# Kernel tuning notes

Hardware: AMD Instinct MI355X
Metric: run time of the kernel (lower is better)

## Reference

```python
import jax, jax.numpy as jnp
import numpy as np

# Sampled-neighborhood cascade sizes (src->dst per layer) and edge counts
N0, N1, N2, N3 = 400000, 200000, 100000, 50000
E1, E2, E3 = 500000, 300000, 150000
DIN, DH = 128, 128


def setup_inputs() -> dict:
    key = jax.random.key(0)
    ks = jax.random.split(key, 24)
    inp = {}
    inp['x'] = jax.random.normal(ks[0], (N0, DIN), jnp.float32)
    inp['src1'] = jax.random.randint(ks[1], (E1,), 0, N0, dtype=jnp.int64)
    inp['dst1'] = jax.random.randint(ks[2], (E1,), 0, N1, dtype=jnp.int64)
    inp['src2'] = jax.random.randint(ks[3], (E2,), 0, N1, dtype=jnp.int64)
    inp['dst2'] = jax.random.randint(ks[4], (E2,), 0, N2, dtype=jnp.int64)
    inp['src3'] = jax.random.randint(ks[5], (E3,), 0, N2, dtype=jnp.int64)
    inp['dst3'] = jax.random.randint(ks[6], (E3,), 0, N3, dtype=jnp.int64)
    # SAGEConv params: lin_l (on aggregated neighbors, with bias), lin_r (root, no bias)
    dims = [(DIN, DH), (DH, DH), (DH, DH)]
    for i, (di, do) in enumerate(dims, start=1):
        s = 1.0 / np.sqrt(di)
        inp[f'Wl{i}'] = jax.random.uniform(ks[6 + 4 * i - 3], (di, do), jnp.float32, -s, s)
        inp[f'Wr{i}'] = jax.random.uniform(ks[6 + 4 * i - 2], (di, do), jnp.float32, -s, s)
        inp[f'b{i}'] = jax.random.uniform(ks[6 + 4 * i - 1], (do,), jnp.float32, -s, s)
        inp[f'a{i}'] = jnp.full((do,), 0.25, jnp.float32)  # PReLU per-channel init
    return inp


def _sage_prelu(x_src, n_dst, src, dst, Wl, Wr, b, alpha):
    # mean aggregation over incoming edges (PyG SAGEConv default aggr='mean')
    x_dst = x_src[:n_dst]                                   # [n_dst, d]
    msg = x_src[src]                                        # [E, d] gather
    summed = jax.ops.segment_sum(msg, dst, num_segments=n_dst)
    cnt = jax.ops.segment_sum(jnp.ones(src.shape[0], x_src.dtype), dst,
                              num_segments=n_dst)
    mean = summed / jnp.maximum(cnt, 1.0)[:, None]
    out = mean @ Wl + b + x_dst @ Wr                        # lin_l(aggr) + lin_r(root)
    return jnp.where(out > 0, out, alpha * out)             # per-channel PReLU


def reference(x, src1, dst1, src2, dst2, src3, dst3,
              Wl1, Wr1, b1, a1, Wl2, Wr2, b2, a2, Wl3, Wr3, b3, a3):
    h = _sage_prelu(x, N1, src1, dst1, Wl1, Wr1, b1, a1)
    h = _sage_prelu(h, N2, src2, dst2, Wl2, Wr2, b2, a2)
    h = _sage_prelu(h, N3, src3, dst3, Wl3, Wr3, b3, a3)
    return h  # [N3, DH]
```

## Files before the change

### kernel.cpp

```cpp
#include <hip/hip_runtime.h>


constexpr int cN0 = 400000, cN1 = 200000, cN2 = 100000, cN3 = 50000;
constexpr int cE1 = 500000, cE2 = 300000, cE3 = 150000;
constexpr int cNT = cN1 + cN2 + cN3;
constexpr int cET = cE1 + cE2 + cE3;

#define NDIV_UP(a, b) (((a) + (b) - 1) / (b))

typedef __attribute__((ext_vector_type(8))) short bf16x8;
typedef __attribute__((ext_vector_type(4))) float f32x4;
typedef __attribute__((ext_vector_type(4))) unsigned u32x4;

__device__ __forceinline__ unsigned fbits(float f) {
  return __builtin_bit_cast(unsigned, f);
}
__device__ __forceinline__ float ffrom(unsigned u) {
  return __builtin_bit_cast(float, u);
}
__device__ __forceinline__ unsigned short f2bf(float f) {
  unsigned u = fbits(f);
  unsigned r = u + 0x7FFFu + ((u >> 16) & 1u);
  return (unsigned short)(r >> 16);
}

__global__ void detect_idx64_kernel(const long long* __restrict__ p, int E,
                                    long long nmax, int* __restrict__ flag) {
  int t = threadIdx.x;
  int n = E < 512 ? E : 512;
  int bad = 0;
  for (int i = t; i < n; i += 64) {
    long long v = p[i];
    if (v < 0 || v >= nmax) bad = 1;
  }
  unsigned long long b = __ballot(bad);
  if (t == 0) *flag = (b == 0ull) ? 1 : 0;
}

__device__ __forceinline__ int load_idx(const void* p, int i, int flag) {
  return flag ? (int)((const long long*)p)[i] : ((const int*)p)[i];
}

constexpr int NBLK_CH = NDIV_UP(cET, 256);

__global__ __launch_bounds__(256) void convhistpack_kernel(
    const float* __restrict__ x, unsigned short* __restrict__ xb,
    const void* __restrict__ d1, const void* __restrict__ d2,
    const void* __restrict__ d3, const int* __restrict__ flag,
    int* __restrict__ CNT,
    const float* __restrict__ Wl1, const float* __restrict__ Wr1,
    const float* __restrict__ Wl2, const float* __restrict__ Wr2,
    const float* __restrict__ Wl3, const float* __restrict__ Wr3,
    unsigned short* __restrict__ wpk) {
  const int bid = blockIdx.x;
  const int tid = threadIdx.x;
  const int gidx = bid * 256 + tid;

  if (gidx < cET) {
    const int f = *flag;
    int d;
    if (gidx < cE1) d = load_idx(d1, gidx, f);
    else if (gidx < cE1 + cE2) d = cN1 + load_idx(d2, gidx - cE1, f);
    else d = cN1 + cN2 + load_idx(d3, gidx - cE1 - cE2, f);
    atomicAdd(&CNT[d], 1);
  }

  {
    const int total4 = cN0 * 128 / 4;
    const int stride = NBLK_CH * 256;
    for (int i = gidx; i < total4; i += stride) {
      const float4 v = ((const float4*)x)[i];
      uint2 o;
      o.x = (unsigned)f2bf(v.x) | ((unsigned)f2bf(v.y) << 16);
      o.y = (unsigned)f2bf(v.z) | ((unsigned)f2bf(v.w) << 16);
      ((uint2*)xb)[i] = o;
    }
  }

  if (gidx < 3 * 16384) {
    const int L = gidx >> 14;
    const int r = gidx & 16383;
    const float* Wl = L == 0 ? Wl1 : (L == 1 ? Wl2 : Wl3);
    const float* Wr = L == 0 ? Wr1 : (L == 1 ? Wr2 : Wr3);
    unsigned short* o = wpk + L * 32768;
    const int j = r & 7, l = (r >> 3) & 63, cf = (r >> 9) & 7, ks = r >> 12;
    const int k = ks * 32 + (l >> 4) * 8 + j;
    const int col = cf * 16 + (l & 15);
    o[r] = f2bf(Wl[k * 128 + col]);
    o[16384 + r] = f2bf(Wr[k * 128 + col]);
  }
}

__global__ __launch_bounds__(256) void scan_reduce(const int* __restrict__ cnt,
                                                   int n, int* __restrict__ bsum) {
  __shared__ int s[256];
  int t = threadIdx.x;
  int base = blockIdx.x * 1024 + t * 4;
  int v = 0;
  if (base + 3 < n) {
    int4 c = *(const int4*)(cnt + base);
    v = c.x + c.y + c.z + c.w;
  } else {
    for (int i = 0; i < 4; ++i)
      if (base + i < n) v += cnt[base + i];
  }
  s[t] = v;
  __syncthreads();
  for (int off = 128; off > 0; off >>= 1) {
    if (t < off) s[t] += s[t + off];
    __syncthreads();
  }
  if (t == 0) bsum[blockIdx.x] = s[0];
}

__global__ __launch_bounds__(256) void scan_bsums(int* __restrict__ bsum, int nb) {
  __shared__ int s[256];
  int t = threadIdx.x;
  int v0 = (2 * t < nb) ? bsum[2 * t] : 0;
  int v1 = (2 * t + 1 < nb) ? bsum[2 * t + 1] : 0;
  int p = v0 + v1;
  s[t] = p;
  __syncthreads();
  for (int off = 1; off < 256; off <<= 1) {
    int x = (t >= off) ? s[t - off] : 0;
    __syncthreads();
    s[t] += x;
    __syncthreads();
  }
  int excl = s[t] - p;
  if (2 * t < nb) bsum[2 * t] = excl;
  if (2 * t + 1 < nb) bsum[2 * t + 1] = excl + v0;
}

__global__ __launch_bounds__(256) void scan_final(const int* __restrict__ cnt,
                                                  int n, const int* __restrict__ bsum,
                                                  int* __restrict__ offs) {
  __shared__ int s[256];
  int t = threadIdx.x;
  int base = blockIdx.x * 1024 + t * 4;
  int v0 = 0, v1 = 0, v2 = 0, v3 = 0;
  if (base + 3 < n) {
    int4 c = *(const int4*)(cnt + base);
    v0 = c.x; v1 = c.y; v2 = c.z; v3 = c.w;
  } else {
    if (base + 0 < n) v0 = cnt[base + 0];
    if (base + 1 < n) v1 = cnt[base + 1];
    if (base + 2 < n) v2 = cnt[base + 2];
  }
  int tsum = v0 + v1 + v2 + v3;
  s[t] = tsum;
  __syncthreads();
  for (int off = 1; off < 256; off <<= 1) {
    int x = (t >= off) ? s[t - off] : 0;
    __syncthreads();
    s[t] += x;
    __syncthreads();
  }
  int excl = s[t] - tsum;
  int o = bsum[blockIdx.x] + excl;
  if (base + 0 < n) offs[base + 0] = o;
  o += v0;
  if (base + 1 < n) offs[base + 1] = o;
  o += v1;
  if (base + 2 < n) offs[base + 2] = o;
  o += v2;
  if (base + 3 < n) offs[base + 3] = o;
}

__global__ void fill3_kernel(const void* __restrict__ s1, const void* __restrict__ d1,
                             const void* __restrict__ s2, const void* __restrict__ d2,
                             const void* __restrict__ s3, const void* __restrict__ d3,
                             const int* __restrict__ flag,
                             int* __restrict__ OFFS, int* __restrict__ EID) {
  int e = blockIdx.x * 256 + threadIdx.x;
  if (e >= cET) return;
  int f = *flag;
  int s, d;
  if (e < cE1) {
    s = load_idx(s1, e, f);
    d = load_idx(d1, e, f);
  } else if (e < cE1 + cE2) {
    int i = e - cE1;
    s = load_idx(s2, i, f);
    d = cN1 + load_idx(d2, i, f);
  } else {
    int i = e - cE1 - cE2;
    s = load_idx(s3, i, f);
    d = cN1 + cN2 + load_idx(d3, i, f);
  }
  int pos = atomicAdd(&OFFS[d], 1);
  EID[pos] = s;
}

__global__ __launch_bounds__(256) void gather_kernel(
    const unsigned short* __restrict__ hsrc, const int* __restrict__ OFFS,
    const int* __restrict__ EID, int rowoff,
    unsigned short* __restrict__ meanB, int n) {
  const int wid = blockIdx.x * 4 + (threadIdx.x >> 6);
  const int lane = threadIdx.x & 63;
  const int r0 = wid * 4;
  if (r0 >= n) return;
  const int gr0 = rowoff + r0;

  int b[5];
  b[0] = (gr0 == 0) ? 0 : OFFS[gr0 - 1];
#pragma unroll
  for (int j = 0; j < 4; ++j)
    b[j + 1] = (r0 + j < n) ? OFFS[gr0 + j] : -1;
#pragma unroll
  for (int j = 0; j < 4; ++j)
    if (b[j + 1] < 0) b[j + 1] = b[j];

  float a0[4] = {0.f, 0.f, 0.f, 0.f};
  float a1[4] = {0.f, 0.f, 0.f, 0.f};

  const int bend = b[4];
  if (bend > b[0]) {
    const int blast = bend - 1;
    for (int e = b[0]; e < bend; e += 8) {
      int sid[8];
#pragma unroll
      for (int k = 0; k < 8; ++k) {
        const int ei = e + k;
        sid[k] = EID[ei <= blast ? ei : blast];
      }
      float v0[8], v1[8];
#pragma unroll
      for (int k = 0; k < 8; ++k) {
        const unsigned u = *(const unsigned*)(hsrc + (size_t)sid[k] * 128 + lane * 2);
        v0[k] = ffrom(u << 16);
        v1[k] = ffrom(u & 0xFFFF0000u);
      }
#pragma unroll
      for (int k = 0; k < 8; ++k) {
        const int ei = e + k;
#pragma unroll
        for (int j = 0; j < 4; ++j) {
          const bool p = (ei >= b[j]) & (ei < b[j + 1]);
          a0[j] += p ? v0[k] : 0.f;
          a1[j] += p ? v1[k] : 0.f;
        }
      }
    }
  }

#pragma unroll
  for (int j = 0; j < 4; ++j) {
    const int row = r0 + j;
    if (row < n) {
      const int cnt = b[j + 1] - b[j];
      const float inv = (cnt > 0) ? 1.0f / (float)cnt : 0.0f;
      const unsigned o = (unsigned)f2bf(a0[j] * inv) |
                         ((unsigned)f2bf(a1[j] * inv) << 16);
      *(unsigned*)(meanB + (size_t)row * 128 + lane * 2) = o;
    }
  }
}

template <bool OUTF32>
__global__ __launch_bounds__(256, 2) void gemm_kernel(
    const unsigned short* __restrict__ meanB,
    const unsigned short* __restrict__ xsrc,
    const unsigned short* __restrict__ W,
    const float* __restrict__ bias, const float* __restrict__ alpha,
    void* __restrict__ outp, int n) {
  __shared__ __align__(16) unsigned short wlds[32768];
  const int tid = threadIdx.x;
  const int lane = tid & 63;
  const int wv = tid >> 6;
  const int rbase = blockIdx.x * 128 + wv * 32;
  const int g = lane >> 4;
  const int r16 = lane & 15;

  bf16x8 am[2][4], ax[2][4];
#pragma unroll
  for (int t = 0; t < 2; ++t) {
    const int row = rbase + t * 16 + r16;
    const bool ok = row < n;
#pragma unroll
    for (int ks = 0; ks < 4; ++ks) {
      if (ok) {
        am[t][ks] = *(const bf16x8*)(meanB + (size_t)row * 128 + ks * 32 + g * 8);
        ax[t][ks] = *(const bf16x8*)(xsrc + (size_t)row * 128 + ks * 32 + g * 8);
      } else {
        am[t][ks] = (bf16x8)0;
        ax[t][ks] = (bf16x8)0;
      }
    }
  }

  {
    const float4* Wg = (const float4*)W;
    float4* Ws = (float4*)wlds;
#pragma unroll
    for (int i = 0; i < 16; ++i)
      Ws[i * 256 + tid] = Wg[i * 256 + tid];
  }
  __syncthreads();

  f32x4 acc[2][8] = {};
#pragma unroll
  for (int ks = 0; ks < 4; ++ks) {
    const unsigned short* wb = wlds + ks * 4096 + lane * 8;
#pragma unroll
    for (int cf = 0; cf < 8; ++cf) {
      const unsigned short* wp = wb + cf * 512;
      bf16x8 wl = *(const bf16x8*)(wp);
      bf16x8 wr = *(const bf16x8*)(wp + 16384);
#pragma unroll
      for (int t = 0; t < 2; ++t) {
        acc[t][cf] = __builtin_amdgcn_mfma_f32_16x16x32_bf16(am[t][ks], wl, acc[t][cf], 0, 0, 0);
        acc[t][cf] = __builtin_amdgcn_mfma_f32_16x16x32_bf16(ax[t][ks], wr, acc[t][cf], 0, 0, 0);
      }
    }
  }

  const int ocol0 = lane & 15;
  const int orow_off = (lane >> 4) * 4;
#pragma unroll
  for (int cf = 0; cf < 8; ++cf) {
    const int ocol = cf * 16 + ocol0;
    const float b = bias[ocol];
    const float a = alpha[ocol];
#pragma unroll
    for (int t = 0; t < 2; ++t) {
      const int orb = rbase + t * 16 + orow_off;
#pragma unroll
      for (int i = 0; i < 4; ++i) {
        const int orow = orb + i;
        if (orow < n) {
          float v = acc[t][cf][i] + b;
          v = v > 0.f ? v : a * v;
          if (OUTF32) {
            ((float*)outp)[(size_t)orow * 128 + ocol] = v;
          } else {
            ((unsigned short*)outp)[(size_t)orow * 128 + ocol] = f2bf(v);
          }
        }
      }
    }
  }
}

extern "C" void kernel_launch(void* const* d_in, const int* in_sizes, int n_in,
                              void* d_out, int out_size, void* d_ws, size_t ws_size,
                              hipStream_t stream) {
  const float* x = (const float*)d_in[0];
  const void* src1 = d_in[1];
  const void* dst1 = d_in[2];
  const void* src2 = d_in[3];
  const void* dst2 = d_in[4];
  const void* src3 = d_in[5];
  const void* dst3 = d_in[6];
  const float* Wl1 = (const float*)d_in[7];
  const float* Wr1 = (const float*)d_in[8];
  const float* b1  = (const float*)d_in[9];
  const float* a1  = (const float*)d_in[10];
  const float* Wl2 = (const float*)d_in[11];
  const float* Wr2 = (const float*)d_in[12];
  const float* b2  = (const float*)d_in[13];
  const float* a2  = (const float*)d_in[14];
  const float* Wl3 = (const float*)d_in[15];
  const float* Wr3 = (const float*)d_in[16];
  const float* b3  = (const float*)d_in[17];
  const float* a3  = (const float*)d_in[18];

  unsigned short* M1 = (unsigned short*)d_ws;
  unsigned short* xb = M1 + (size_t)cN1 * 128;
  unsigned short* M2 = xb;
  unsigned short* M3 = xb + (size_t)cN2 * 128;
  int* CNT = (int*)(xb + (size_t)cN0 * 128);
  int* OFFS = CNT + cNT;
  int* EID = OFFS + cNT;
  int* bsum = EID + cET;
  int* flag = bsum + 1024;
  unsigned short* wpk = (unsigned short*)(flag + 64);

  const int nb = NDIV_UP(cNT, 1024);

  detect_idx64_kernel<<<1, 64, 0, stream>>>((const long long*)src1, cE1,
                                            (long long)cN0, flag);
  hipMemsetAsync(CNT, 0, (size_t)cNT * sizeof(int), stream);
  convhistpack_kernel<<<NBLK_CH, 256, 0, stream>>>(
      x, xb, dst1, dst2, dst3, flag, CNT,
      Wl1, Wr1, Wl2, Wr2, Wl3, Wr3, wpk);
  scan_reduce<<<nb, 256, 0, stream>>>(CNT, cNT, bsum);
  scan_bsums<<<1, 256, 0, stream>>>(bsum, nb);
  scan_final<<<nb, 256, 0, stream>>>(CNT, cNT, bsum, OFFS);
  fill3_kernel<<<NDIV_UP(cET, 256), 256, 0, stream>>>(src1, dst1, src2, dst2,
                                                      src3, dst3, flag, OFFS, EID);

  gather_kernel<<<NDIV_UP(cN1, 16), 256, 0, stream>>>(
      xb, OFFS, EID, 0, M1, cN1);
  gemm_kernel<false><<<NDIV_UP(cN1, 128), 256, 0, stream>>>(
      M1, xb, wpk, b1, a1, M1, cN1);

  gather_kernel<<<NDIV_UP(cN2, 16), 256, 0, stream>>>(
      M1, OFFS, EID, cN1, M2, cN2);
  gemm_kernel<false><<<NDIV_UP(cN2, 128), 256, 0, stream>>>(
      M2, M1, wpk + 32768, b2, a2, M2, cN2);

  gather_kernel<<<NDIV_UP(cN3, 16), 256, 0, stream>>>(
      M2, OFFS, EID, cN1 + cN2, M3, cN3);
  gemm_kernel<true><<<NDIV_UP(cN3, 128), 256, 0, stream>>>(
      M3, M2, wpk + 65536, b3, a3, d_out, cN3);
}
```

Measured before the change: 352.9 us.

## Split fused conv/histogram/pack kernel into separate kernels, replace memset with zero kernel

The fused kernel that converted x to bf16, built the destination histogram and packed the weights is split into three kernels. The x conversion now runs after the CSR build as its own grid-stride kernel with 2048 blocks, and hipMemsetAsync is replaced by a small zero kernel. The intent is to stop the atomic histogram and the bulk conversion from competing inside one launch, and to avoid memset overhead. In exchange it adds several kernel launches and loses any overlap the fused version had.

```diff
diff --git a/kernel.cpp b/kernel.cpp
--- a/kernel.cpp
+++ b/kernel.cpp
@@ -22,6 +22,24 @@
   unsigned u = fbits(f);
   unsigned r = u + 0x7FFFu + ((u >> 16) & 1u);
   return (unsigned short)(r >> 16);
+}
+
+__global__ __launch_bounds__(256) void zero_kernel(int4* __restrict__ p, int n4) {
+  int i = blockIdx.x * 256 + threadIdx.x;
+  if (i < n4) p[i] = make_int4(0, 0, 0, 0);
+}
+
+__global__ __launch_bounds__(256) void conv_kernel(const float* __restrict__ x,
+                                                   unsigned short* __restrict__ xb) {
+  const int total4 = cN0 * 128 / 4;
+  const int stride = gridDim.x * 256;
+  for (int i = blockIdx.x * 256 + threadIdx.x; i < total4; i += stride) {
+    const float4 v = ((const float4*)x)[i];
+    uint2 o;
+    o.x = (unsigned)f2bf(v.x) | ((unsigned)f2bf(v.y) << 16);
+    o.y = (unsigned)f2bf(v.z) | ((unsigned)f2bf(v.w) << 16);
+    ((uint2*)xb)[i] = o;
+  }
 }
 
 __global__ void detect_idx64_kernel(const long long* __restrict__ p, int E,
@@ -41,54 +59,17 @@
   return flag ? (int)((const long long*)p)[i] : ((const int*)p)[i];
 }
 
-constexpr int NBLK_CH = NDIV_UP(cET, 256);
-
-__global__ __launch_bounds__(256) void convhistpack_kernel(
-    const float* __restrict__ x, unsigned short* __restrict__ xb,
-    const void* __restrict__ d1, const void* __restrict__ d2,
-    const void* __restrict__ d3, const int* __restrict__ flag,
-    int* __restrict__ CNT,
-    const float* __restrict__ Wl1, const float* __restrict__ Wr1,
-    const float* __restrict__ Wl2, const float* __restrict__ Wr2,
-    const float* __restrict__ Wl3, const float* __restrict__ Wr3,
-    unsigned short* __restrict__ wpk) {
-  const int bid = blockIdx.x;
-  const int tid = threadIdx.x;
-  const int gidx = bid * 256 + tid;
-
-  if (gidx < cET) {
-    const int f = *flag;
-    int d;
-    if (gidx < cE1) d = load_idx(d1, gidx, f);
-    else if (gidx < cE1 + cE2) d = cN1 + load_idx(d2, gidx - cE1, f);
-    else d = cN1 + cN2 + load_idx(d3, gidx - cE1 - cE2, f);
-    atomicAdd(&CNT[d], 1);
-  }
-
-  {
-    const int total4 = cN0 * 128 / 4;
-    const int stride = NBLK_CH * 256;
-    for (int i = gidx; i < total4; i += stride) {
-      const float4 v = ((const float4*)x)[i];
-      uint2 o;
-      o.x = (unsigned)f2bf(v.x) | ((unsigned)f2bf(v.y) << 16);
-      o.y = (unsigned)f2bf(v.z) | ((unsigned)f2bf(v.w) << 16);
-      ((uint2*)xb)[i] = o;
-    }
-  }
-
-  if (gidx < 3 * 16384) {
-    const int L = gidx >> 14;
-    const int r = gidx & 16383;
-    const float* Wl = L == 0 ? Wl1 : (L == 1 ? Wl2 : Wl3);
-    const float* Wr = L == 0 ? Wr1 : (L == 1 ? Wr2 : Wr3);
-    unsigned short* o = wpk + L * 32768;
-    const int j = r & 7, l = (r >> 3) & 63, cf = (r >> 9) & 7, ks = r >> 12;
-    const int k = ks * 32 + (l >> 4) * 8 + j;
-    const int col = cf * 16 + (l & 15);
-    o[r] = f2bf(Wl[k * 128 + col]);
-    o[16384 + r] = f2bf(Wr[k * 128 + col]);
-  }
+__global__ void hist3_kernel(const void* __restrict__ d1, const void* __restrict__ d2,
+                             const void* __restrict__ d3, const int* __restrict__ flag,
+                             int* __restrict__ CNT) {
+  int e = blockIdx.x * 256 + threadIdx.x;
+  if (e >= cET) return;
+  int f = *flag;
+  int d;
+  if (e < cE1) d = load_idx(d1, e, f);
+  else if (e < cE1 + cE2) d = cN1 + load_idx(d2, e - cE1, f);
+  else d = cN1 + cN2 + load_idx(d3, e - cE1 - cE2, f);
+  atomicAdd(&CNT[d], 1);
 }
 
 __global__ __launch_bounds__(256) void scan_reduce(const int* __restrict__ cnt,
@@ -190,6 +171,24 @@
   }
   int pos = atomicAdd(&OFFS[d], 1);
   EID[pos] = s;
+}
+
+__global__ void pack_w3_kernel(const float* __restrict__ Wl1, const float* __restrict__ Wr1,
+                               const float* __restrict__ Wl2, const float* __restrict__ Wr2,
+                               const float* __restrict__ Wl3, const float* __restrict__ Wr3,
+                               unsigned short* __restrict__ wpk) {
+  int idx = blockIdx.x * 256 + threadIdx.x;
+  if (idx >= 3 * 16384) return;
+  int L = idx >> 14;
+  int r = idx & 16383;
+  const float* Wl = L == 0 ? Wl1 : (L == 1 ? Wl2 : Wl3);
+  const float* Wr = L == 0 ? Wr1 : (L == 1 ? Wr2 : Wr3);
+  unsigned short* o = wpk + L * 32768;
+  int j = r & 7, l = (r >> 3) & 63, cf = (r >> 9) & 7, ks = r >> 12;
+  int k = ks * 32 + (l >> 4) * 8 + j;
+  int col = cf * 16 + (l & 15);
+  o[r] = f2bf(Wl[k * 128 + col]);
+  o[16384 + r] = f2bf(Wr[k * 128 + col]);
 }
 
 __global__ __launch_bounds__(256) void gather_kernel(
@@ -380,16 +379,17 @@
 
   detect_idx64_kernel<<<1, 64, 0, stream>>>((const long long*)src1, cE1,
                                             (long long)cN0, flag);
-  hipMemsetAsync(CNT, 0, (size_t)cNT * sizeof(int), stream);
-  convhistpack_kernel<<<NBLK_CH, 256, 0, stream>>>(
-      x, xb, dst1, dst2, dst3, flag, CNT,
-      Wl1, Wr1, Wl2, Wr2, Wl3, Wr3, wpk);
+  pack_w3_kernel<<<192, 256, 0, stream>>>(Wl1, Wr1, Wl2, Wr2, Wl3, Wr3, wpk);
+  zero_kernel<<<NDIV_UP(cNT / 4, 256), 256, 0, stream>>>((int4*)CNT, cNT / 4);
+  hist3_kernel<<<NDIV_UP(cET, 256), 256, 0, stream>>>(dst1, dst2, dst3, flag, CNT);
   scan_reduce<<<nb, 256, 0, stream>>>(CNT, cNT, bsum);
   scan_bsums<<<1, 256, 0, stream>>>(bsum, nb);
   scan_final<<<nb, 256, 0, stream>>>(CNT, cNT, bsum, OFFS);
   fill3_kernel<<<NDIV_UP(cET, 256), 256, 0, stream>>>(src1, dst1, src2, dst2,
                                                       src3, dst3, flag, OFFS, EID);
 
+  conv_kernel<<<2048, 256, 0, stream>>>(x, xb);
+
   gather_kernel<<<NDIV_UP(cN1, 16), 256, 0, stream>>>(
       xb, OFFS, EID, 0, M1, cN1);
   gemm_kernel<false><<<NDIV_UP(cN1, 128), 256, 0, stream>>>(
```

Result: slower. 380.7 us (+7.9%).
